# Optimization experiments

Hardware: AMD Instinct MI355X
Metric: run time of the kernel (lower is better)

Reference implementation:

```python
import jax, jax.numpy as jnp
import numpy as np

B, N, D, S, NH, ITERS, MLP_H = 64, 4096, 256, 8, 8, 3, 512
DK = D // NH
EPS = 1e-5


def _layernorm(x, g, b):
    m = jnp.mean(x, axis=-1, keepdims=True)
    v = jnp.mean((x - m) ** 2, axis=-1, keepdims=True)
    return (x - m) / jnp.sqrt(v + EPS) * g + b


def setup_inputs() -> dict:
    key = jax.random.key(0)
    ks = jax.random.split(key, 24)
    w = lambda k, shp: jax.random.normal(k, shp, dtype=jnp.float32) * 0.02
    return {
        "inputs": jax.random.normal(ks[0], (B, N, D), dtype=jnp.float32),
        "noise": jax.random.normal(ks[1], (B, S, D), dtype=jnp.float32),
        "slots_mu": jax.random.normal(ks[2], (1, 1, D), dtype=jnp.float32),
        "slots_log_sigma": jax.random.normal(ks[3], (1, 1, D), dtype=jnp.float32) * 0.1,
        "wq": w(ks[4], (D, D)), "bq": jnp.zeros((D,), jnp.float32),
        "wk": w(ks[5], (D, D)), "bk": jnp.zeros((D,), jnp.float32),
        "wv": w(ks[6], (D, D)), "bv": jnp.zeros((D,), jnp.float32),
        "wo": w(ks[7], (D, D)), "bo": jnp.zeros((D,), jnp.float32),
        "w_ih": w(ks[8], (3 * D, D)), "b_ih": jnp.zeros((3 * D,), jnp.float32),
        "w_hh": w(ks[9], (3 * D, D)), "b_hh": jnp.zeros((3 * D,), jnp.float32),
        "mlp_w1": w(ks[10], (D, MLP_H)), "mlp_b1": jnp.zeros((MLP_H,), jnp.float32),
        "mlp_w2": w(ks[11], (MLP_H, D)), "mlp_b2": jnp.zeros((D,), jnp.float32),
        "g_in": jnp.ones((D,), jnp.float32), "b_in": jnp.zeros((D,), jnp.float32),
        "g_slot": jnp.ones((D,), jnp.float32), "b_slot": jnp.zeros((D,), jnp.float32),
        "g_mlp": jnp.ones((D,), jnp.float32), "b_mlp": jnp.zeros((D,), jnp.float32),
    }


def reference(inputs, noise, slots_mu, slots_log_sigma,
              wq, bq, wk, bk, wv, bv, wo, bo,
              w_ih, b_ih, w_hh, b_hh,
              mlp_w1, mlp_b1, mlp_w2, mlp_b2,
              g_in, b_in, g_slot, b_slot, g_mlp, b_mlp):
    b, n, d = inputs.shape
    s = noise.shape[1]
    # slot init: mu + exp(log_sigma) * noise
    slots = slots_mu + jnp.exp(slots_log_sigma) * noise  # [B,S,D]
    x = _layernorm(inputs, g_in, b_in)
    # K/V depend only on normed inputs -> hoist out of the loop (same math)
    K = (x @ wk + bk).reshape(b, n, NH, DK).transpose(0, 2, 1, 3)  # [B,H,N,DK]
    V = (x @ wv + bv).reshape(b, n, NH, DK).transpose(0, 2, 1, 3)
    scale = 1.0 / jnp.sqrt(jnp.float32(DK))
    for _ in range(ITERS):
        sp = _layernorm(slots, g_slot, b_slot)
        Q = (sp @ wq + bq).reshape(b, s, NH, DK).transpose(0, 2, 1, 3)  # [B,H,S,DK]
        scores = jnp.einsum("bhsd,bhnd->bhsn", Q, K) * scale
        attn = jax.nn.softmax(scores, axis=-1)
        out = jnp.einsum("bhsn,bhnd->bhsd", attn, V)
        out = out.transpose(0, 2, 1, 3).reshape(b, s, d) @ wo + bo
        # GRUCell(input=out, hidden=slots), PyTorch semantics
        xi = out.reshape(-1, d)
        h = slots.reshape(-1, d)
        gi = xi @ w_ih.T + b_ih
        gh = h @ w_hh.T + b_hh
        i_r, i_z, i_n = jnp.split(gi, 3, axis=-1)
        h_r, h_z, h_n = jnp.split(gh, 3, axis=-1)
        r = jax.nn.sigmoid(i_r + h_r)
        z = jax.nn.sigmoid(i_z + h_z)
        ng = jnp.tanh(i_n + r * h_n)
        slots = ((1.0 - z) * ng + z * h).reshape(b, s, d)
        # residual MLP
        m = _layernorm(slots, g_mlp, b_mlp)
        slots = slots + jax.nn.relu(m @ mlp_w1 + mlp_b1) @ mlp_w2 + mlp_b2
    return slots
```

## Files before the change

### kernel.cpp

```cpp
#include <hip/hip_runtime.h>
#include <hip/hip_bf16.h>

#define B_ 64
#define N_ 4096
#define D_ 256
#define S_ 8
#define NH_ 8
#define DK_ 32
#define ITERS_ 3
#define MLPH_ 512
#define EPS_ 1e-5f
#define M_ (B_*N_)
#define NEG_BIG_ -3.0e38f
#define NSPLIT_ 4

typedef unsigned short u16;
typedef short bf16x8 __attribute__((ext_vector_type(8)));
typedef float f32x4 __attribute__((ext_vector_type(4)));

__device__ __forceinline__ u16 f2bf(float f){
  unsigned int x = __float_as_uint(f);
  return (u16)((x + 0x7fffu + ((x >> 16) & 1u)) >> 16);
}
__device__ __forceinline__ unsigned int pkbf(float a, float b){
  return (unsigned int)f2bf(a) | ((unsigned int)f2bf(b) << 16);
}

__global__ void prep_kernel(const float* __restrict__ wk, const float* __restrict__ wv,
                            const float* __restrict__ wih, const float* __restrict__ whh,
                            u16* __restrict__ wkvT, float* __restrict__ wihT,
                            float* __restrict__ whhT){
  int idx = blockIdx.x * 256 + threadIdx.x;
  if(idx < 512*256){
    int n = idx >> 8, k = idx & 255;
    float v = (n < 256) ? wk[k*256 + n] : wv[k*256 + (n-256)];
    wkvT[n*256 + k] = f2bf(v);
    return;
  }
  int i2 = idx - 512*256;
  if(i2 < 196608){
    int d = i2 / 768, j = i2 - d*768;
    wihT[i2] = wih[j*256 + d];
    return;
  }
  int i3 = i2 - 196608;
  if(i3 < 196608){
    int d = i3 / 768, j = i3 - d*768;
    whhT[i3] = whh[j*256 + d];
  }
}

__global__ void init_slots(const float* __restrict__ mu, const float* __restrict__ lsig,
                           const float* __restrict__ noise, float* __restrict__ slots){
  int idx = blockIdx.x * 256 + threadIdx.x;
  int d = idx & 255;
  slots[idx] = mu[d] + __expf(lsig[d]) * noise[idx];
}

__global__ __launch_bounds__(256) void ln_kernel(const float* __restrict__ inp,
                                                 const float* __restrict__ g,
                                                 const float* __restrict__ b,
                                                 u16* __restrict__ xb){
  int wave = threadIdx.x >> 6, lane = threadIdx.x & 63;
  int row = blockIdx.x * 4 + wave;
  float4 v = *(const float4*)(inp + (size_t)row*D_ + lane*4);
  float s  = v.x+v.y+v.z+v.w;
  float ss = v.x*v.x + v.y*v.y + v.z*v.z + v.w*v.w;
  #pragma unroll
  for(int o=32;o>=1;o>>=1){ s += __shfl_xor(s,o,64); ss += __shfl_xor(ss,o,64); }
  float mean = s * (1.f/D_);
  float var  = ss * (1.f/D_) - mean*mean;
  float rstd = rsqrtf(var + EPS_);
  float4 gg = *(const float4*)(g + lane*4);
  float4 bb = *(const float4*)(b + lane*4);
  ushort4 o4;
  o4.x = f2bf((v.x-mean)*rstd*gg.x + bb.x);
  o4.y = f2bf((v.y-mean)*rstd*gg.y + bb.y);
  o4.z = f2bf((v.z-mean)*rstd*gg.z + bb.z);
  o4.w = f2bf((v.w-mean)*rstd*gg.w + bb.w);
  *(ushort4*)(xb + (size_t)row*D_ + lane*4) = o4;
}

__global__ __launch_bounds__(512) void kv_gemm(const u16* __restrict__ xb,
                                               const u16* __restrict__ wkvT,
                                               const float* __restrict__ bk,
                                               const float* __restrict__ bv,
                                               u16* __restrict__ Kp, u16* __restrict__ Vp){
  __shared__ u16 As[64*256];
  int rt = blockIdx.x;
  int tid = threadIdx.x;
  int w = tid >> 6, lane = tid & 63;
  int lr = lane & 15, quad = lane >> 4;

  {
    const u16* agp = xb + (size_t)(rt*64)*256;
    int i0 = w*4;
    #pragma unroll
    for(int i=0;i<4;i++){
      int r = 2*(i0+i) + (lane >> 5);
      int c16 = lane & 31;
      __builtin_amdgcn_global_load_lds(
        (const __attribute__((address_space(1))) void*)(agp + (size_t)r*256 + ((c16 ^ (r&7)) << 3)),
        (__attribute__((address_space(3))) void*)(As + (i0+i)*512),
        16, 0, 0);
    }
  }

  f32x4 zf = {0.f,0.f,0.f,0.f};
  f32x4 acc[4][4];
  #pragma unroll
  for(int mt=0;mt<4;mt++)
    #pragma unroll
    for(int nt=0;nt<4;nt++) acc[mt][nt] = zf;

  const u16* bw = wkvT + (size_t)(w*64)*256;

  __syncthreads();

  #pragma unroll 2
  for(int kc=0; kc<8; kc++){
    bf16x8 a[4], b[4];
    #pragma unroll
    for(int mt=0;mt<4;mt++){
      int R = mt*16 + lr;
      int chunk = kc*4 + quad;
      int sw = (chunk & 0x18) | ((chunk ^ R) & 7);
      a[mt] = *(const bf16x8*)(As + R*256 + sw*8);
    }
    #pragma unroll
    for(int nt=0;nt<4;nt++)
      b[nt] = *(const bf16x8*)(bw + (size_t)(nt*16 + lr)*256 + kc*32 + quad*8);
    #pragma unroll
    for(int mt=0;mt<4;mt++)
      #pragma unroll
      for(int nt=0;nt<4;nt++)
        acc[mt][nt] = __builtin_amdgcn_mfma_f32_16x16x32_bf16(a[mt], b[nt], acc[mt][nt], 0,0,0);
  }

  #pragma unroll
  for(int mt=0;mt<4;mt++){
    #pragma unroll
    for(int nt=0;nt<4;nt++){
      int gc = w*64 + nt*16 + lr;
      int gr0 = rt*64 + mt*16 + quad*4;
      #pragma unroll
      for(int i=0;i<4;i++){
        int gr = gr0 + i;
        int bb = gr >> 12, n = gr & 4095;
        float v = acc[mt][nt][i];
        if(gc < 256){
          int h = gc >> 5, d = gc & 31;
          Kp[((size_t)(bb*8 + h)*4096 + n)*32 + d] = f2bf(v + bk[gc]);
        } else {
          int c2 = gc - 256;
          int h = c2 >> 5, d = c2 & 31;
          Vp[((size_t)(bb*8 + h)*32 + d)*4096 + n] = f2bf(v + bv[c2]);
        }
      }
    }
  }
}

__global__ __launch_bounds__(256) void qproj(const float* __restrict__ slots,
                                             const float* __restrict__ g,
                                             const float* __restrict__ b,
                                             const float* __restrict__ wq,
                                             const float* __restrict__ bq,
                                             float* __restrict__ Q){
  __shared__ float sp[256];
  __shared__ float red[8];
  int r = blockIdx.x, t = threadIdx.x;
  float v = slots[r*256 + t];
  float s1 = v, s2 = v*v;
  #pragma unroll
  for(int o=32;o>=1;o>>=1){ s1 += __shfl_xor(s1,o,64); s2 += __shfl_xor(s2,o,64); }
  int wv_ = t >> 6, lane = t & 63;
  if(lane==0){ red[wv_] = s1; red[4+wv_] = s2; }
  __syncthreads();
  float fs1 = red[0]+red[1]+red[2]+red[3];
  float fs2 = red[4]+red[5]+red[6]+red[7];
  float mean = fs1*(1.f/256.f);
  float var  = fs2*(1.f/256.f) - mean*mean;
  float rstd = rsqrtf(var + EPS_);
  sp[t] = (v - mean)*rstd*g[t] + b[t];
  __syncthreads();
  float acc = bq[t];
  for(int d=0; d<256; d++) acc = fmaf(sp[d], wq[d*256 + t], acc);
  int b_ = r >> 3, s_ = r & 7;
  int h = t >> 5, d_ = t & 31;
  Q[((b_*8 + h)*8 + s_)*32 + d_] = acc;
}

__global__ __launch_bounds__(256) void attn_part(const float* __restrict__ Qw,
                                                 const u16* __restrict__ Kp,
                                                 const u16* __restrict__ Vp,
                                                 float2* __restrict__ Pml,
                                                 float* __restrict__ Po){
  const int bh = blockIdx.x, sp_ = blockIdx.y;
  const int w = threadIdx.x >> 6, lane = threadIdx.x & 63;
  const int c = lane & 15, q = lane >> 4;
  const float scale = 0.17677669529663687f;

  __shared__ float oW[4][8][32];
  __shared__ float mW[4][8], lW[4][8];

  bf16x8 qf;
  {
    union { u16 u[8]; bf16x8 v; } qq;
    if(c < 8){
      const float4* qp = (const float4*)(Qw + ((size_t)bh*8 + c)*32 + q*8);
      float4 v0 = qp[0], v1 = qp[1];
      qq.u[0]=f2bf(v0.x); qq.u[1]=f2bf(v0.y); qq.u[2]=f2bf(v0.z); qq.u[3]=f2bf(v0.w);
      qq.u[4]=f2bf(v1.x); qq.u[5]=f2bf(v1.y); qq.u[6]=f2bf(v1.z); qq.u[7]=f2bf(v1.w);
    } else {
      #pragma unroll
      for(int e=0;e<8;e++) qq.u[e]=0;
    }
    qf = qq.v;
  }

  const int row0 = sp_*(N_/NSPLIT_) + w*(N_/NSPLIT_/4);
  const u16* kb = Kp + (size_t)bh*(N_*DK_) + (size_t)row0*DK_;
  const u16* vt = Vp + (size_t)bh*(N_*DK_) + row0;

  float m = NEG_BIG_, l = 0.f;
  f32x4 acc2[2] = {{0.f,0.f,0.f,0.f},{0.f,0.f,0.f,0.f}};
  const int La = c + 32*(q&1);
  const int Lb = La + 16;
  const int thi = q >> 1;

  #pragma unroll 2
  for(int ch=0; ch<8; ch++){
    bf16x8 kf0 = *(const bf16x8*)(kb + (size_t)(ch*32 +      c)*DK_ + q*8);
    bf16x8 kf1 = *(const bf16x8*)(kb + (size_t)(ch*32 + 16 + c)*DK_ + q*8);
    bf16x8 vf0 = *(const bf16x8*)(vt + (size_t)(     c)*N_ + ch*32 + q*8);
    bf16x8 vf1 = *(const bf16x8*)(vt + (size_t)(16 + c)*N_ + ch*32 + q*8);

    f32x4 s0 = {0.f,0.f,0.f,0.f}, s1 = {0.f,0.f,0.f,0.f};
    s0 = __builtin_amdgcn_mfma_f32_16x16x32_bf16(kf0, qf, s0, 0,0,0);
    s1 = __builtin_amdgcn_mfma_f32_16x16x32_bf16(kf1, qf, s1, 0,0,0);

    float p[8];
    #pragma unroll
    for(int r=0;r<4;r++){ p[r] = s0[r]*scale; p[4+r] = s1[r]*scale; }
    float cm = p[0];
    #pragma unroll
    for(int i=1;i<8;i++) cm = fmaxf(cm, p[i]);
    cm = fmaxf(cm, __shfl_xor(cm, 16, 64));
    cm = fmaxf(cm, __shfl_xor(cm, 32, 64));
    float nm = fmaxf(m, cm);
    float corr = __expf(m - nm);
    m = nm;
    float ps = 0.f;
    #pragma unroll
    for(int i=0;i<8;i++){ p[i] = __expf(p[i] - nm); ps += p[i]; }
    ps += __shfl_xor(ps, 16, 64);
    ps += __shfl_xor(ps, 32, 64);
    l = l*corr + ps;
    #pragma unroll
    for(int r=0;r<4;r++){ acc2[0][r] *= corr; acc2[1][r] *= corr; }

    unsigned int u0 = pkbf(p[0],p[1]), u1 = pkbf(p[2],p[3]);
    unsigned int u2 = pkbf(p[4],p[5]), u3 = pkbf(p[6],p[7]);
    unsigned int a0 = (unsigned int)__shfl((int)u0, La, 64);
    unsigned int a1 = (unsigned int)__shfl((int)u1, La, 64);
    unsigned int a2 = (unsigned int)__shfl((int)u2, La, 64);
    unsigned int a3 = (unsigned int)__shfl((int)u3, La, 64);
    unsigned int b0 = (unsigned int)__shfl((int)u0, Lb, 64);
    unsigned int b1 = (unsigned int)__shfl((int)u1, Lb, 64);
    unsigned int b2 = (unsigned int)__shfl((int)u2, Lb, 64);
    unsigned int b3 = (unsigned int)__shfl((int)u3, Lb, 64);
    union { unsigned int wu[4]; bf16x8 v; } pf;
    pf.wu[0] = thi ? a2 : a0;
    pf.wu[1] = thi ? a3 : a1;
    pf.wu[2] = thi ? b2 : b0;
    pf.wu[3] = thi ? b3 : b1;

    acc2[0] = __builtin_amdgcn_mfma_f32_16x16x32_bf16(vf0, pf.v, acc2[0], 0,0,0);
    acc2[1] = __builtin_amdgcn_mfma_f32_16x16x32_bf16(vf1, pf.v, acc2[1], 0,0,0);
  }

  if(c < 8){
    #pragma unroll
    for(int t=0;t<2;t++)
      #pragma unroll
      for(int r=0;r<4;r++)
        oW[w][c][16*t + 4*q + r] = acc2[t][r];
    if(q == 0){ mW[w][c] = m; lW[w][c] = l; }
  }
  __syncthreads();
  {
    int s = threadIdx.x >> 5, d = threadIdx.x & 31;
    float M = fmaxf(fmaxf(mW[0][s], mW[1][s]), fmaxf(mW[2][s], mW[3][s]));
    float L = 0.f, O = 0.f;
    #pragma unroll
    for(int k=0;k<4;k++){
      float e = __expf(mW[k][s] - M);
      L += lW[k][s]*e;
      O += oW[k][s][d]*e;
    }
    Po[((size_t)(bh*8 + s)*NSPLIT_ + sp_)*32 + d] = O;
    if(d == 0) Pml[(bh*8 + s)*NSPLIT_ + sp_] = make_float2(M, L);
  }
}

__global__ __launch_bounds__(256) void attn_merge(const float2* __restrict__ Pml,
                                                  const float* __restrict__ Po,
                                                  float* __restrict__ Ow){
  int gid = blockIdx.x * 256 + threadIdx.x;
  int row = gid >> 5, d = gid & 31;
  float2 ml[NSPLIT_];
  #pragma unroll
  for(int k=0;k<NSPLIT_;k++) ml[k] = Pml[row*NSPLIT_ + k];
  float M = ml[0].x;
  #pragma unroll
  for(int k=1;k<NSPLIT_;k++) M = fmaxf(M, ml[k].x);
  float L = 0.f, o = 0.f;
  #pragma unroll
  for(int k=0;k<NSPLIT_;k++){
    float e = __expf(ml[k].x - M);
    L += ml[k].y * e;
    o += Po[(size_t)(row*NSPLIT_ + k)*32 + d] * e;
  }
  Ow[row*32 + d] = o / L;
}

__global__ __launch_bounds__(256) void gru_mlp(const float* __restrict__ Ain,
    const float* __restrict__ slots_in,
    const float* __restrict__ wo,  const float* __restrict__ bo,
    const float* __restrict__ wihT,const float* __restrict__ bih,
    const float* __restrict__ whhT,const float* __restrict__ bhh,
    const float* __restrict__ w1,  const float* __restrict__ b1,
    const float* __restrict__ w2,  const float* __restrict__ b2,
    const float* __restrict__ gm,  const float* __restrict__ bm,
    float* __restrict__ slots_out){
  __shared__ float xr[4][256], hr[4][256], o2[4][256], hnew[4][256], hid[4][512];
  __shared__ float red[4][8];
  int t = threadIdx.x, r0 = blockIdx.x*4;
  int wv_ = t >> 6, lane = t & 63;
  #pragma unroll
  for(int rr=0;rr<4;rr++){
    int r = r0+rr, b_ = r>>3, s_ = r&7;
    int h = t>>5, d = t&31;
    xr[rr][t] = Ain[((b_*8 + h)*8 + s_)*32 + d];
    hr[rr][t] = slots_in[r*256 + t];
  }
  __syncthreads();
  {
    float a0=0,a1=0,a2=0,a3=0;
    for(int d=0; d<256; d++){
      float w = wo[d*256 + t];
      a0 = fmaf(xr[0][d],w,a0); a1 = fmaf(xr[1][d],w,a1);
      a2 = fmaf(xr[2][d],w,a2); a3 = fmaf(xr[3][d],w,a3);
    }
    float bv = bo[t];
    o2[0][t]=a0+bv; o2[1][t]=a1+bv; o2[2][t]=a2+bv; o2[3][t]=a3+bv;
  }
  __syncthreads();
  {
    float ir[4]={}, iz[4]={}, inn[4]={}, hrr[4]={}, hz[4]={}, hn[4]={};
    for(int d=0; d<256; d++){
      float wi0 = wihT[d*768 + t], wi1 = wihT[d*768 + 256 + t], wi2 = wihT[d*768 + 512 + t];
      float wh0 = whhT[d*768 + t], wh1 = whhT[d*768 + 256 + t], wh2 = whhT[d*768 + 512 + t];
      #pragma unroll
      for(int rr=0;rr<4;rr++){
        float xo = o2[rr][d], hh = hr[rr][d];
        ir[rr]  = fmaf(xo,wi0,ir[rr]);  iz[rr] = fmaf(xo,wi1,iz[rr]);  inn[rr] = fmaf(xo,wi2,inn[rr]);
        hrr[rr] = fmaf(hh,wh0,hrr[rr]); hz[rr] = fmaf(hh,wh1,hz[rr]);  hn[rr]  = fmaf(hh,wh2,hn[rr]);
      }
    }
    float bi0 = bih[t], bi1 = bih[256+t], bi2 = bih[512+t];
    float bh0 = bhh[t], bh1 = bhh[256+t], bh2 = bhh[512+t];
    #pragma unroll
    for(int rr=0;rr<4;rr++){
      float rg = 1.f/(1.f + __expf(-(ir[rr]+bi0 + hrr[rr]+bh0)));
      float zg = 1.f/(1.f + __expf(-(iz[rr]+bi1 + hz[rr]+bh1)));
      float ng = tanhf(inn[rr]+bi2 + rg*(hn[rr]+bh2));
      hnew[rr][t] = (1.f - zg)*ng + zg*hr[rr][t];
    }
  }
  __syncthreads();
  #pragma unroll
  for(int rr=0;rr<4;rr++){
    float v = hnew[rr][t];
    float s1=v, s2=v*v;
    #pragma unroll
    for(int o=32;o>=1;o>>=1){ s1 += __shfl_xor(s1,o,64); s2 += __shfl_xor(s2,o,64); }
    if(lane==0){ red[rr][wv_]=s1; red[rr][4+wv_]=s2; }
  }
  __syncthreads();
  {
    float gmt = gm[t], bmt = bm[t];
    #pragma unroll
    for(int rr=0;rr<4;rr++){
      float fs1 = red[rr][0]+red[rr][1]+red[rr][2]+red[rr][3];
      float fs2 = red[rr][4]+red[rr][5]+red[rr][6]+red[rr][7];
      float mean = fs1*(1.f/256.f);
      float var  = fs2*(1.f/256.f) - mean*mean;
      float rstd = rsqrtf(var + EPS_);
      xr[rr][t] = (hnew[rr][t]-mean)*rstd*gmt + bmt;
    }
  }
  __syncthreads();
  {
    float c0[4]={}, c1[4]={};
    for(int d=0; d<256; d++){
      float wA = w1[d*512 + t], wB = w1[d*512 + 256 + t];
      #pragma unroll
      for(int rr=0;rr<4;rr++){ float mv = xr[rr][d]; c0[rr]=fmaf(mv,wA,c0[rr]); c1[rr]=fmaf(mv,wB,c1[rr]); }
    }
    float b1a = b1[t], b1b = b1[256+t];
    #pragma unroll
    for(int rr=0;rr<4;rr++){
      hid[rr][t]     = fmaxf(c0[rr]+b1a, 0.f);
      hid[rr][t+256] = fmaxf(c1[rr]+b1b, 0.f);
    }
  }
  __syncthreads();
  {
    float a[4]={};
    for(int k=0;k<512;k++){
      float w = w2[k*256 + t];
      #pragma unroll
      for(int rr=0;rr<4;rr++) a[rr] = fmaf(hid[rr][k], w, a[rr]);
    }
    float b2t = b2[t];
    #pragma unroll
    for(int rr=0;rr<4;rr++){
      int r = r0+rr;
      slots_out[r*256 + t] = hnew[rr][t] + a[rr] + b2t;
    }
  }
}

extern "C" void kernel_launch(void* const* d_in, const int* in_sizes, int n_in,
                              void* d_out, int out_size, void* d_ws, size_t ws_size,
                              hipStream_t stream){
  const float* inputs = (const float*)d_in[0];
  const float* noise  = (const float*)d_in[1];
  const float* mu     = (const float*)d_in[2];
  const float* lsig   = (const float*)d_in[3];
  const float* wq  = (const float*)d_in[4];  const float* bq  = (const float*)d_in[5];
  const float* wk  = (const float*)d_in[6];  const float* bk  = (const float*)d_in[7];
  const float* wv  = (const float*)d_in[8];  const float* bv  = (const float*)d_in[9];
  const float* wo  = (const float*)d_in[10]; const float* bo  = (const float*)d_in[11];
  const float* wih = (const float*)d_in[12]; const float* bih = (const float*)d_in[13];
  const float* whh = (const float*)d_in[14]; const float* bhh = (const float*)d_in[15];
  const float* w1  = (const float*)d_in[16]; const float* b1  = (const float*)d_in[17];
  const float* w2  = (const float*)d_in[18]; const float* b2  = (const float*)d_in[19];
  const float* g_in= (const float*)d_in[20]; const float* b_in= (const float*)d_in[21];
  const float* g_sl= (const float*)d_in[22]; const float* b_sl= (const float*)d_in[23];
  const float* g_ml= (const float*)d_in[24]; const float* b_ml= (const float*)d_in[25];

  const size_t sz_big = (size_t)M_ * D_ * 2;
  size_t need = 3*sz_big + 512*256*2 + 2*(256*768*4) + 3*(512*256*4)
              + 4096*NSPLIT_*8 + (size_t)4096*NSPLIT_*32*4;
  if(ws_size < need) return;

  char* p = (char*)d_ws;
  u16*   xb   = (u16*)p;   p += sz_big;
  u16*   Kp   = (u16*)p;   p += sz_big;
  u16*   Vp   = (u16*)p;   p += sz_big;
  u16*   wkvT = (u16*)p;   p += 512*256*2;
  float* wihT = (float*)p; p += 256*768*4;
  float* whhT = (float*)p; p += 256*768*4;
  float* slots= (float*)p; p += 512*256*4;
  float* Qw   = (float*)p; p += 512*256*4;
  float* Ow   = (float*)p; p += 512*256*4;
  float2* Pml = (float2*)p; p += 4096*NSPLIT_*8;
  float* Po   = (float*)p;  p += (size_t)4096*NSPLIT_*32*4;

  prep_kernel<<<2048, 256, 0, stream>>>(wk, wv, wih, whh, wkvT, wihT, whhT);
  init_slots <<<512, 256, 0, stream>>>(mu, lsig, noise, slots);
  ln_kernel  <<<M_/4, 256, 0, stream>>>(inputs, g_in, b_in, xb);
  kv_gemm    <<<M_/64, 512, 0, stream>>>(xb, wkvT, bk, bv, Kp, Vp);

  for(int it = 0; it < ITERS_; ++it){
    qproj<<<512, 256, 0, stream>>>(slots, g_sl, b_sl, wq, bq, Qw);
    attn_part<<<dim3(512, NSPLIT_), 256, 0, stream>>>(Qw, Kp, Vp, Pml, Po);
    attn_merge<<<512, 256, 0, stream>>>(Pml, Po, Ow);
    float* outp = (it == ITERS_-1) ? (float*)d_out : slots;
    gru_mlp<<<128, 256, 0, stream>>>(Ow, slots, wo, bo, wihT, bih, whhT, bhh,
                                     w1, b1, w2, b2, g_ml, b_ml, outp);
  }
}
```

Baseline: 1.193 ms.

## Double-buffer weight loads and stage transposed V output through LDS

In the K/V projection kernel, weight fragments for the next k-chunk are now prefetched into alternating register buffers while the current chunk's MFMAs run, and the k loop is fully unrolled. The V output, which is stored transposed (n contiguous), is first written to a swizzled LDS tile and then copied out with 16-byte coalesced stores instead of scattered 2-byte global writes. K stores are restructured but remain scalar. This adds register pressure and an extra LDS round trip with two barriers.

```diff
diff --git a/kernel.cpp b/kernel.cpp
--- a/kernel.cpp
+++ b/kernel.cpp
@@ -115,11 +115,23 @@
 
   const u16* bw = wkvT + (size_t)(w*64)*256;
 
-  __syncthreads();
-
-  #pragma unroll 2
+  bf16x8 bA[4], bB[4];
+  #pragma unroll
+  for(int nt=0;nt<4;nt++)
+    bA[nt] = *(const bf16x8*)(bw + (size_t)(nt*16 + lr)*256 + quad*8);
+
+  __syncthreads();
+
+  #pragma unroll
   for(int kc=0; kc<8; kc++){
-    bf16x8 a[4], b[4];
+    if(kc < 7){
+      #pragma unroll
+      for(int nt=0;nt<4;nt++){
+        bf16x8 nb = *(const bf16x8*)(bw + (size_t)(nt*16 + lr)*256 + (kc+1)*32 + quad*8);
+        if(kc & 1) bA[nt] = nb; else bB[nt] = nb;
+      }
+    }
+    bf16x8 a[4];
     #pragma unroll
     for(int mt=0;mt<4;mt++){
       int R = mt*16 + lr;
@@ -128,35 +140,60 @@
       a[mt] = *(const bf16x8*)(As + R*256 + sw*8);
     }
     #pragma unroll
-    for(int nt=0;nt<4;nt++)
-      b[nt] = *(const bf16x8*)(bw + (size_t)(nt*16 + lr)*256 + kc*32 + quad*8);
-    #pragma unroll
     for(int mt=0;mt<4;mt++)
       #pragma unroll
       for(int nt=0;nt<4;nt++)
-        acc[mt][nt] = __builtin_amdgcn_mfma_f32_16x16x32_bf16(a[mt], b[nt], acc[mt][nt], 0,0,0);
-  }
-
-  #pragma unroll
-  for(int mt=0;mt<4;mt++){
+        acc[mt][nt] = __builtin_amdgcn_mfma_f32_16x16x32_bf16(
+            a[mt], (kc & 1) ? bB[nt] : bA[nt], acc[mt][nt], 0,0,0);
+  }
+
+  const int bb = rt >> 6;
+  const int n0 = (rt & 63) * 64;
+  u16* T = As;
+
+  __syncthreads();
+
+  if(w >= 4){
     #pragma unroll
     for(int nt=0;nt<4;nt++){
-      int gc = w*64 + nt*16 + lr;
-      int gr0 = rt*64 + mt*16 + quad*4;
-      #pragma unroll
-      for(int i=0;i<4;i++){
-        int gr = gr0 + i;
-        int bb = gr >> 12, n = gr & 4095;
-        float v = acc[mt][nt][i];
-        if(gc < 256){
-          int h = gc >> 5, d = gc & 31;
-          Kp[((size_t)(bb*8 + h)*4096 + n)*32 + d] = f2bf(v + bk[gc]);
-        } else {
-          int c2 = gc - 256;
-          int h = c2 >> 5, d = c2 & 31;
-          Vp[((size_t)(bb*8 + h)*32 + d)*4096 + n] = f2bf(v + bv[c2]);
+      int d_ = (w-4)*64 + nt*16 + lr;
+      float bias = bv[d_];
+      int d7 = (d_ & 7) << 3;
+      #pragma unroll
+      for(int mt=0;mt<4;mt++){
+        #pragma unroll
+        for(int i=0;i<4;i++){
+          int n = mt*16 + quad*4 + i;
+          T[d_*64 + (n ^ d7)] = f2bf(acc[mt][nt][i] + bias);
         }
       }
+    }
+  } else {
+    #pragma unroll
+    for(int mt=0;mt<4;mt++){
+      #pragma unroll
+      for(int nt=0;nt<4;nt++){
+        int gc = w*64 + nt*16 + lr;
+        int h = gc >> 5, d = gc & 31;
+        float bias = bk[gc];
+        #pragma unroll
+        for(int i=0;i<4;i++){
+          int n = n0 + mt*16 + quad*4 + i;
+          Kp[((size_t)(bb*8 + h)*4096 + n)*32 + d] = f2bf(acc[mt][nt][i] + bias);
+        }
+      }
+    }
+  }
+  __syncthreads();
+  {
+    int d2 = tid >> 1, half = tid & 1;
+    int h = d2 >> 5, d = d2 & 31;
+    int d7 = d2 & 7;
+    u16* dst = Vp + ((size_t)(bb*8 + h)*32 + d)*4096 + n0 + half*32;
+    #pragma unroll
+    for(int j=0;j<4;j++){
+      int c = half*4 + j;
+      *(uint4*)(dst + j*8) = *(const uint4*)(T + d2*64 + ((c ^ d7) << 3));
     }
   }
 }
```

Result: faster. 1.108 ms (-7.1%).
